# Kernel tuning notes

Hardware: AMD Instinct MI355X
Metric: run time of the kernel (lower is better)

The kernel has to match this reference:

```python
import jax, jax.numpy as jnp
import numpy as np
import math

B, L, D, H = 16, 512, 128, 8


def setup_inputs() -> dict:
    key = jax.random.key(0)
    ks = jax.random.split(key, 10)
    xavier = lambda k, shp: jax.random.normal(k, shp, jnp.float32) * math.sqrt(2.0 / (shp[0] + shp[1]))
    inp = {
        "x": jax.random.normal(ks[0], (B, L, D), jnp.float32),
        "W_q": xavier(ks[1], (H * D, D)),
        "b_q": jnp.zeros((H * D,), jnp.float32),
        "W_k": xavier(ks[2], (H * D, D)),
        "b_k": jnp.zeros((H * D,), jnp.float32),
        "W_v": xavier(ks[3], (H * D, D)),
        "b_v": jnp.zeros((H * D,), jnp.float32),
        "W_o": xavier(ks[4], (D, H * D)),
        "b_o": jnp.zeros((D,), jnp.float32),
        "pad_mask": jax.random.randint(ks[5], (B, L, L), 0, 2).astype(bool),
        "batch_size": B,
        "max_len": L,
    }
    return inp


def reference(x, W_q, b_q, W_k, b_k, W_v, b_v, W_o, b_o, pad_mask, batch_size, max_len):
    # project: [B, L, D] -> [B, L, H*D] -> head-major [H*B, L, D]
    def proj(W, b):
        y = jnp.einsum('bld,ed->ble', x, W) + b          # [B, L, H*D]
        y = y.reshape(batch_size, max_len, H, D)
        return y.transpose(2, 0, 1, 3).reshape(H * batch_size, max_len, D)

    q = proj(W_q, b_q)
    k = proj(W_k, b_k)
    v = proj(W_v, b_v)

    scores = jnp.einsum('nqd,nkd->nqk', q, k)            # [H*B, L, L]
    mask = jnp.tile(pad_mask, (H, 1, 1))                 # repeat(n_heads,1,1)
    # faithful quirk: mask BEFORE scaling, softmax over QUERY axis (dim=1)
    scores = jnp.where(mask, -1e9, scores) / math.sqrt(D)
    attn = jax.nn.softmax(scores, axis=1)
    att = jnp.einsum('nqk,nkd->nqd', attn, v)            # [H*B, L, D]
    # faithful quirk: torch .view from (H*B, L, D) to (B, L, H*D)
    att = att.reshape(batch_size, max_len, H * D)
    out = jnp.einsum('ble,de->bld', att, W_o) + b_o      # [B, L, D]
    return out
```

## Files before the change

### kernel.cpp

```cpp
#include <hip/hip_runtime.h>

#define B_  16
#define L_  512
#define D_  128
#define H_  8
#define HD_ 1024
#define NH_ 128
#define M_  8192

typedef unsigned short u16;
typedef __attribute__((ext_vector_type(8))) short s16x8;
typedef __attribute__((ext_vector_type(4))) float f32x4;

__device__ __forceinline__ float bf2f(u16 u) {
    union { unsigned u; float f; } x; x.u = ((unsigned)u) << 16; return x.f;
}
__device__ __forceinline__ u16 f2bf(float f) {
    unsigned u = __float_as_uint(f);
    return (u16)((u + 0x7FFFu + ((u >> 16) & 1u)) >> 16);
}

template<int MI, int MJ>
__device__ __forceinline__ void mfma_bt(const u16* __restrict__ A, int lda,
                                        const u16* __restrict__ B, int ldb,
                                        int K, int lane, f32x4 acc[MI][MJ]) {
    const int mr = lane & 15, quad = lane >> 4;
    for (int k0 = 0; k0 < K; k0 += 32) {
        s16x8 av[MI], bv[MJ];
#pragma unroll
        for (int i = 0; i < MI; i++)
            av[i] = *(const s16x8*)(A + (size_t)(i * 16 + mr) * lda + k0 + quad * 8);
#pragma unroll
        for (int j = 0; j < MJ; j++)
            bv[j] = *(const s16x8*)(B + (size_t)(j * 16 + mr) * ldb + k0 + quad * 8);
#pragma unroll
        for (int i = 0; i < MI; i++)
#pragma unroll
            for (int j = 0; j < MJ; j++)
                acc[i][j] = __builtin_amdgcn_mfma_f32_16x16x32_bf16(av[i], bv[j], acc[i][j], 0, 0, 0);
    }
}

__global__ void k0_detect(const unsigned int* __restrict__ pad,
                          const unsigned int* __restrict__ xw,
                          int* __restrict__ flags) {
    __shared__ int sMask, sCnt;
    if (threadIdx.x == 0) { sMask = 0; sCnt = 0; }
    __syncthreads();
    int bad = 0;
#pragma unroll
    for (int i = 0; i < 4; i++) {
        unsigned u = pad[threadIdx.x * 4 + i];
        bad |= (u > 1u) ? 1 : 0;
    }
    int cnt = 0;
#pragma unroll
    for (int i = 0; i < 16; i++) {
        unsigned w = xw[threadIdx.x * 16 + i];
        unsigned e = (w >> 7) & 0xFFu;
        cnt += (e >= 100u && e <= 131u) ? 1 : 0;
    }
    if (bad) atomicOr(&sMask, 1);
    atomicAdd(&sCnt, cnt);
    __syncthreads();
    if (threadIdx.x == 0) {
        flags[0] = (sCnt > 2048) ? 1 : 0;
        flags[1] = sMask;
    }
}

#define PREP_G8 197008
__global__ __launch_bounds__(256) void kprep_conv8(
    const void* x, const void* Wq, const void* bq, const void* Wk, const void* bk,
    const void* Wv, const void* bv, const void* Wo, const void* bo,
    const int* __restrict__ flags,
    u16* xb, u16* Wqb, u16* Wkb, u16* Wvb, u16* Wob,
    u16* bqb, u16* bkb, u16* bvb, u16* bob) {
    int g = blockIdx.x * 256 + threadIdx.x;
    if (g >= PREP_G8) return;
    int e0 = g * 8;
    const int dt = flags[0];
    const void* src; u16* dst; int off;
    if      (e0 < 1048576) { src = x;  dst = xb;  off = e0; }
    else if (e0 < 1179648) { src = Wq; dst = Wqb; off = e0 - 1048576; }
    else if (e0 < 1310720) { src = Wk; dst = Wkb; off = e0 - 1179648; }
    else if (e0 < 1441792) { src = Wv; dst = Wvb; off = e0 - 1310720; }
    else if (e0 < 1572864) { src = Wo; dst = Wob; off = e0 - 1441792; }
    else if (e0 < 1573888) { src = bq; dst = bqb; off = e0 - 1572864; }
    else if (e0 < 1574912) { src = bk; dst = bkb; off = e0 - 1573888; }
    else if (e0 < 1575936) { src = bv; dst = bvb; off = e0 - 1574912; }
    else                   { src = bo; dst = bob; off = e0 - 1575936; }
    if (dt) {
        *(uint4*)(dst + off) = *(const uint4*)((const u16*)src + off);
    } else {
        float4 a = *(const float4*)((const float*)src + off);
        float4 b = *(const float4*)((const float*)src + off + 4);
        u16 t[8] = {f2bf(a.x), f2bf(a.y), f2bf(a.z), f2bf(a.w),
                    f2bf(b.x), f2bf(b.y), f2bf(b.z), f2bf(b.w)};
        *(uint4*)(dst + off) = *(const uint4*)t;
    }
}

__global__ __launch_bounds__(256) void kprep_mask(const void* __restrict__ pad,
                                                  const int* __restrict__ flags,
                                                  unsigned* __restrict__ mb,
                                                  float* __restrict__ lsum) {
    int w = blockIdx.x * 256 + threadIdx.x;
    if (w < 65536) lsum[w] = 0.f;
    unsigned m = 0;
    if (flags[1]) {
        union { uint4 v[2]; unsigned a[8]; } u;
        u.v[0] = ((const uint4*)pad)[w * 2];
        u.v[1] = ((const uint4*)pad)[w * 2 + 1];
#pragma unroll
        for (int b = 0; b < 32; b++)
            m |= (((u.a[b >> 2] >> ((b & 3) * 8)) & 0xFFu) ? 1u : 0u) << b;
    } else {
        union { uint4 v[8]; unsigned a[32]; } u;
#pragma unroll
        for (int i = 0; i < 8; i++) u.v[i] = ((const uint4*)pad)[w * 8 + i];
#pragma unroll
        for (int b = 0; b < 32; b++) m |= (u.a[b] ? 1u : 0u) << b;
    }
    mb[w] = m;
}

__global__ __launch_bounds__(256) void k1_proj(
    const u16* __restrict__ xb,
    const u16* __restrict__ Wqb, const u16* __restrict__ Wkb, const u16* __restrict__ Wvb,
    const u16* __restrict__ bqb, const u16* __restrict__ bkb, const u16* __restrict__ bvb,
    u16* __restrict__ qb, u16* __restrict__ kb, u16* __restrict__ vtb) {
    const int h  = blockIdx.x;
    const int m0 = blockIdx.y * 128;
    const int z  = blockIdx.z;
    const u16* W    = (z == 0) ? Wqb : (z == 1) ? Wkb : Wvb;
    const u16* bias = (z == 0) ? bqb : (z == 1) ? bkb : bvb;

    const int lane = threadIdx.x & 63, wave = threadIdx.x >> 6;
    const int wr = wave >> 1, wc = wave & 1;
    const int mr = lane & 15, quad = lane >> 4;

    f32x4 acc[4][4];
#pragma unroll
    for (int i = 0; i < 4; i++)
#pragma unroll
        for (int j = 0; j < 4; j++) acc[i][j] = (f32x4){0.f, 0.f, 0.f, 0.f};

    mfma_bt<4,4>(xb + (size_t)(m0 + wr * 64) * D_, D_,
                 W + (size_t)(h * 128 + wc * 64) * D_, D_, D_, lane, acc);

    __shared__ __align__(16) u16 T[128][136];
#pragma unroll
    for (int i = 0; i < 4; i++)
#pragma unroll
        for (int j = 0; j < 4; j++) {
            int col = wc * 64 + j * 16 + mr;
            float bv_ = bf2f(bias[h * 128 + col]);
#pragma unroll
            for (int r = 0; r < 4; r++)
                T[wr * 64 + i * 16 + quad * 4 + r][col] = f2bf(acc[i][j][r] + bv_);
        }
    __syncthreads();

    const int bb = m0 >> 9, l0 = m0 & 511;
    const int t = threadIdx.x;
    if (z < 2) {
        u16* out = z ? kb : qb;
        int row = t >> 1, c0 = (t & 1) * 64;
        u16* dst = out + ((size_t)(h * B_ + bb) * L_ + l0 + row) * D_ + c0;
#pragma unroll
        for (int c = 0; c < 64; c += 8)
            *(uint4*)(dst + c) = *(const uint4*)&T[row][c0 + c];
    } else {
        int d = t >> 1, lc0 = (t & 1) * 64;
        u16* dst = vtb + ((size_t)(h * B_ + bb) * D_ + d) * L_ + l0 + lc0;
#pragma unroll
        for (int c = 0; c < 64; c += 8) {
            u16 tmp[8];
#pragma unroll
            for (int s = 0; s < 8; s++) tmp[s] = T[lc0 + c + s][d];
            *(uint4*)(dst + c) = *(const uint4*)tmp;
        }
    }
}

__global__ __launch_bounds__(256) void k2_escore(
    const u16* __restrict__ qb, const u16* __restrict__ kb,
    const unsigned* __restrict__ mbits,
    u16* __restrict__ E, float* __restrict__ lsum) {
    const int n  = blockIdx.x;
    const int ks = blockIdx.y;
    const int qq = blockIdx.z;
    const int bb = n & (B_ - 1);
    const int tid = threadIdx.x;
    const int lane = tid & 63, wave = tid >> 6;
    const int wr = wave >> 1, wc = wave & 1;
    const int mr = lane & 15, quad = lane >> 4;
    const float rs = 0.08838834764831845f;

    __shared__ __align__(16) u16 Te[128][136];
    __shared__ unsigned mw[512];
    __shared__ float CS[2][128];

#pragma unroll
    for (int s = 0; s < 2; s++) {
        int idx = tid * 2 + s;
        int ql = idx >> 2, lw = idx & 3;
        mw[idx] = mbits[((size_t)(bb << 9) + qq * 128 + ql) * 16 + ks * 4 + lw];
    }
    __syncthreads();

    f32x4 acc[4][4];
#pragma unroll
    for (int i = 0; i < 4; i++)
#pragma unroll
        for (int j = 0; j < 4; j++) acc[i][j] = (f32x4){0.f, 0.f, 0.f, 0.f};

    mfma_bt<4,4>(qb + (size_t)n * L_ * D_ + (size_t)(qq * 128 + wr * 64) * D_, D_,
                 kb + (size_t)n * L_ * D_ + (size_t)(ks * 128 + wc * 64) * D_, D_,
                 D_, lane, acc);

    float colsum[4] = {0.f, 0.f, 0.f, 0.f};
#pragma unroll
    for (int j = 0; j < 4; j++) {
        const int kc = wc * 64 + j * 16 + mr;
        const int lw = kc >> 5, bit = kc & 31;
#pragma unroll
        for (int i = 0; i < 4; i++)
#pragma unroll
            for (int r = 0; r < 4; r++) {
                int ql = wr * 64 + i * 16 + quad * 4 + r;
                float e = ((mw[(ql << 2) + lw] >> bit) & 1u)
                          ? 0.f : __expf(acc[i][j][r] * rs);
                colsum[j] += e;
                Te[ql][kc] = f2bf(e);
            }
    }
#pragma unroll
    for (int j = 0; j < 4; j++) {
        colsum[j] += __shfl_xor(colsum[j], 16);
        colsum[j] += __shfl_xor(colsum[j], 32);
    }
    if (quad == 0) {
#pragma unroll
        for (int j = 0; j < 4; j++) CS[wr][wc * 64 + j * 16 + mr] = colsum[j];
    }
    __syncthreads();

    {
        int row = tid >> 1, c0 = (tid & 1) * 64;
        u16* dst = E + ((size_t)(n * L_ + qq * 128 + row)) * L_ + ks * 128 + c0;
#pragma unroll
        for (int c = 0; c < 64; c += 8)
            *(uint4*)(dst + c) = *(const uint4*)&Te[row][c0 + c];
    }
    if (tid < 128)
        atomicAdd(&lsum[(size_t)n * L_ + ks * 128 + tid], CS[0][tid] + CS[1][tid]);
}

__global__ __launch_bounds__(256) void k3_vscale(u16* __restrict__ vtb,
                                                 const float* __restrict__ lsum) {
    int idx = blockIdx.x * 256 + threadIdx.x;
    int n = idx >> 13;
    int rem = idx & 8191;
    int d = rem >> 6;
    int kg = (rem & 63) << 3;
    u16* p = vtb + ((size_t)n * D_ + d) * L_ + kg;
    uint4 v = *(const uint4*)p;
    float4 l0 = *(const float4*)(lsum + (size_t)n * L_ + kg);
    float4 l1 = *(const float4*)(lsum + (size_t)n * L_ + kg + 4);
    float lv[8] = {1.f/l0.x, 1.f/l0.y, 1.f/l0.z, 1.f/l0.w,
                   1.f/l1.x, 1.f/l1.y, 1.f/l1.z, 1.f/l1.w};
    u16* u = (u16*)&v;
#pragma unroll
    for (int s = 0; s < 8; s++) u[s] = f2bf(bf2f(u[s]) * lv[s]);
    *(uint4*)p = v;
}

__global__ __launch_bounds__(256) void k4_av(
    const u16* __restrict__ E, const u16* __restrict__ vtb,
    u16* __restrict__ att) {
    const int n  = blockIdx.x;
    const int qt = blockIdx.y;
    const int tid = threadIdx.x;
    const int lane = tid & 63, w = tid >> 6;
    const int mr = lane & 15, quad = lane >> 4;

    f32x4 acc[4][2];
#pragma unroll
    for (int i = 0; i < 4; i++)
#pragma unroll
        for (int j = 0; j < 2; j++) acc[i][j] = (f32x4){0.f, 0.f, 0.f, 0.f};

    mfma_bt<4,2>(E + ((size_t)n * L_ + qt * 64) * L_, L_,
                 vtb + ((size_t)n * D_ + w * 32) * L_, L_, L_, lane, acc);

    __shared__ __align__(16) u16 Ta[64][136];
#pragma unroll
    for (int i = 0; i < 4; i++)
#pragma unroll
        for (int j = 0; j < 2; j++) {
            int col = w * 32 + j * 16 + mr;
#pragma unroll
            for (int r = 0; r < 4; r++)
                Ta[i * 16 + quad * 4 + r][col] = f2bf(acc[i][j][r]);
        }
    __syncthreads();
    int row = tid >> 2, c0 = (tid & 3) * 32;
    u16* dst = att + ((size_t)(n * L_ + qt * 64 + row)) * D_ + c0;
#pragma unroll
    for (int c = 0; c < 32; c += 8)
        *(uint4*)(dst + c) = *(const uint4*)&Ta[row][c0 + c];
}

__global__ __launch_bounds__(256) void k5_out(
    const u16* __restrict__ att, const u16* __restrict__ Wob,
    const u16* __restrict__ bob, const int* __restrict__ flags,
    void* __restrict__ out) {
    const int dt = flags[0];
    const int n0 = blockIdx.x * 64;
    const int m0 = blockIdx.y * 32;
    const int tid = threadIdx.x;
    const int lane = tid & 63, wk = tid >> 6;
    const int mr = lane & 15, quad = lane >> 4;

    f32x4 acc[2][4];
#pragma unroll
    for (int i = 0; i < 2; i++)
#pragma unroll
        for (int j = 0; j < 4; j++) acc[i][j] = (f32x4){0.f, 0.f, 0.f, 0.f};

    mfma_bt<2,4>(att + (size_t)m0 * HD_ + wk * 256, HD_,
                 Wob + (size_t)n0 * HD_ + wk * 256, HD_, 256, lane, acc);

    __shared__ __align__(16) float Tf[2][32][68];
    if (wk < 2) {
#pragma unroll
        for (int i = 0; i < 2; i++)
#pragma unroll
            for (int j = 0; j < 4; j++)
#pragma unroll
                for (int r = 0; r < 4; r++)
                    Tf[wk][i * 16 + quad * 4 + r][j * 16 + mr] = acc[i][j][r];
    }
    __syncthreads();
    if (wk >= 2) {
#pragma unroll
        for (int i = 0; i < 2; i++)
#pragma unroll
            for (int j = 0; j < 4; j++)
#pragma unroll
                for (int r = 0; r < 4; r++)
                    Tf[wk - 2][i * 16 + quad * 4 + r][j * 16 + mr] += acc[i][j][r];
    }
    __syncthreads();

    int row = tid >> 3, c0 = (tid & 7) * 8;
    size_t base = (size_t)(m0 + row) * D_ + n0 + c0;
    float v[8];
#pragma unroll
    for (int s = 0; s < 8; s++)
        v[s] = Tf[0][row][c0 + s] + Tf[1][row][c0 + s] + bf2f(bob[n0 + c0 + s]);
    if (dt) {
        u16 tmp[8];
#pragma unroll
        for (int s = 0; s < 8; s++) tmp[s] = f2bf(v[s]);
        *(uint4*)((u16*)out + base) = *(const uint4*)tmp;
    } else {
        float* o = (float*)out;
        *(float4*)(o + base)     = *(const float4*)&v[0];
        *(float4*)(o + base + 4) = *(const float4*)&v[4];
    }
}

extern "C" void kernel_launch(void* const* d_in, const int* in_sizes, int n_in,
                              void* d_out, int out_size, void* d_ws, size_t ws_size,
                              hipStream_t stream) {
    (void)in_sizes; (void)n_in; (void)out_size; (void)ws_size;
    const void* x  = d_in[0];
    const void* Wq = d_in[1]; const void* bq = d_in[2];
    const void* Wk = d_in[3]; const void* bk = d_in[4];
    const void* Wv = d_in[5]; const void* bv = d_in[6];
    const void* Wo = d_in[7]; const void* bo = d_in[8];
    const void* pad = d_in[9];

    char* p = (char*)d_ws;
    auto alloc = [&](size_t bytes) { char* r = p; p += (bytes + 255) & ~(size_t)255; return r; };
    int*  flags = (int*)alloc(256);
    u16*  xb   = (u16*)alloc(2097152);
    u16*  Wqb  = (u16*)alloc(262144);
    u16*  Wkb  = (u16*)alloc(262144);
    u16*  Wvb  = (u16*)alloc(262144);
    u16*  Wob  = (u16*)alloc(262144);
    u16*  bqb  = (u16*)alloc(2048);
    u16*  bkb  = (u16*)alloc(2048);
    u16*  bvb  = (u16*)alloc(2048);
    u16*  bob  = (u16*)alloc(256);
    unsigned* mbits = (unsigned*)alloc(524288);
    float* lsum = (float*)alloc(262144);
    u16*  qb   = (u16*)alloc(16777216);
    u16*  kb   = (u16*)alloc(16777216);
    u16*  vtb  = (u16*)alloc(16777216);
    u16*  E    = (u16*)alloc(67108864);
    u16*  att  = qb;

    k0_detect<<<1, 256, 0, stream>>>((const unsigned*)pad, (const unsigned*)x, flags);
    kprep_conv8<<<(PREP_G8 + 255) / 256, 256, 0, stream>>>(
        x, Wq, bq, Wk, bk, Wv, bv, Wo, bo, flags,
        xb, Wqb, Wkb, Wvb, Wob, bqb, bkb, bvb, bob);
    kprep_mask<<<512, 256, 0, stream>>>(pad, flags, mbits, lsum);
    k1_proj<<<dim3(8, 64, 3), 256, 0, stream>>>(
        xb, Wqb, Wkb, Wvb, bqb, bkb, bvb, qb, kb, vtb);
    k2_escore<<<dim3(128, 4, 4), 256, 0, stream>>>(qb, kb, mbits, E, lsum);
    k3_vscale<<<4096, 256, 0, stream>>>(vtb, lsum);
    k4_av<<<dim3(128, 8), 256, 0, stream>>>(E, vtb, att);
    k5_out<<<dim3(2, 256), 256, 0, stream>>>(att, Wob, bob, flags, d_out);
}
```

Baseline: 263.3 us.

## Fuse input conversion into GEMMs, fold V scaling into AV, shrink blocks

Drops the separate fp32-to-bf16 prep kernel and converts x and the weights on the fly inside the projection and output GEMM fragment loads. Removes the V rescale pass and applies 1/colsum inside the AV kernel via a shared reciprocal table. Resizes k1, k2 and k4 to single-wave 64-thread blocks with smaller tiles and larger grids, and k2 now accumulates column sums directly with atomics. The aim is fewer launches and less intermediate traffic. The cost is repeated conversion work per tile and more atomics.

```diff
diff --git a/kernel.cpp b/kernel.cpp
--- a/kernel.cpp
+++ b/kernel.cpp
@@ -19,20 +19,36 @@
     unsigned u = __float_as_uint(f);
     return (u16)((u + 0x7FFFu + ((u >> 16) & 1u)) >> 16);
 }
+__device__ __forceinline__ float ld1(const void* p, size_t i, int dt) {
+    if (dt) return bf2f(((const u16*)p)[i]);
+    return ((const float*)p)[i];
+}
+
+__device__ __forceinline__ s16x8 ld_frag(const void* p, size_t off, int dt) {
+    if (dt) return *(const s16x8*)((const u16*)p + off);
+    const float* f = (const float*)p + off;
+    float4 a = *(const float4*)f;
+    float4 b = *(const float4*)(f + 4);
+    union { u16 u[8]; s16x8 v; } t;
+    t.u[0] = f2bf(a.x); t.u[1] = f2bf(a.y); t.u[2] = f2bf(a.z); t.u[3] = f2bf(a.w);
+    t.u[4] = f2bf(b.x); t.u[5] = f2bf(b.y); t.u[6] = f2bf(b.z); t.u[7] = f2bf(b.w);
+    return t.v;
+}
 
 template<int MI, int MJ>
-__device__ __forceinline__ void mfma_bt(const u16* __restrict__ A, int lda,
-                                        const u16* __restrict__ B, int ldb,
-                                        int K, int lane, f32x4 acc[MI][MJ]) {
+__device__ __forceinline__ void mfma_core(
+    const void* __restrict__ A, size_t offA, int lda, int dtA,
+    const void* __restrict__ B, size_t offB, int ldb, int dtB,
+    int K, int lane, f32x4 acc[MI][MJ]) {
     const int mr = lane & 15, quad = lane >> 4;
     for (int k0 = 0; k0 < K; k0 += 32) {
         s16x8 av[MI], bv[MJ];
 #pragma unroll
         for (int i = 0; i < MI; i++)
-            av[i] = *(const s16x8*)(A + (size_t)(i * 16 + mr) * lda + k0 + quad * 8);
+            av[i] = ld_frag(A, offA + (size_t)(i * 16 + mr) * lda + k0 + quad * 8, dtA);
 #pragma unroll
         for (int j = 0; j < MJ; j++)
-            bv[j] = *(const s16x8*)(B + (size_t)(j * 16 + mr) * ldb + k0 + quad * 8);
+            bv[j] = ld_frag(B, offB + (size_t)(j * 16 + mr) * ldb + k0 + quad * 8, dtB);
 #pragma unroll
         for (int i = 0; i < MI; i++)
 #pragma unroll
@@ -66,38 +82,6 @@
     if (threadIdx.x == 0) {
         flags[0] = (sCnt > 2048) ? 1 : 0;
         flags[1] = sMask;
-    }
-}
-
-#define PREP_G8 197008
-__global__ __launch_bounds__(256) void kprep_conv8(
-    const void* x, const void* Wq, const void* bq, const void* Wk, const void* bk,
-    const void* Wv, const void* bv, const void* Wo, const void* bo,
-    const int* __restrict__ flags,
-    u16* xb, u16* Wqb, u16* Wkb, u16* Wvb, u16* Wob,
-    u16* bqb, u16* bkb, u16* bvb, u16* bob) {
-    int g = blockIdx.x * 256 + threadIdx.x;
-    if (g >= PREP_G8) return;
-    int e0 = g * 8;
-    const int dt = flags[0];
-    const void* src; u16* dst; int off;
-    if      (e0 < 1048576) { src = x;  dst = xb;  off = e0; }
-    else if (e0 < 1179648) { src = Wq; dst = Wqb; off = e0 - 1048576; }
-    else if (e0 < 1310720) { src = Wk; dst = Wkb; off = e0 - 1179648; }
-    else if (e0 < 1441792) { src = Wv; dst = Wvb; off = e0 - 1310720; }
-    else if (e0 < 1572864) { src = Wo; dst = Wob; off = e0 - 1441792; }
-    else if (e0 < 1573888) { src = bq; dst = bqb; off = e0 - 1572864; }
-    else if (e0 < 1574912) { src = bk; dst = bkb; off = e0 - 1573888; }
-    else if (e0 < 1575936) { src = bv; dst = bvb; off = e0 - 1574912; }
-    else                   { src = bo; dst = bob; off = e0 - 1575936; }
-    if (dt) {
-        *(uint4*)(dst + off) = *(const uint4*)((const u16*)src + off);
-    } else {
-        float4 a = *(const float4*)((const float*)src + off);
-        float4 b = *(const float4*)((const float*)src + off + 4);
-        u16 t[8] = {f2bf(a.x), f2bf(a.y), f2bf(a.z), f2bf(a.w),
-                    f2bf(b.x), f2bf(b.y), f2bf(b.z), f2bf(b.w)};
-        *(uint4*)(dst + off) = *(const uint4*)t;
     }
 }
 
@@ -125,19 +109,20 @@
     mb[w] = m;
 }
 
-__global__ __launch_bounds__(256) void k1_proj(
-    const u16* __restrict__ xb,
-    const u16* __restrict__ Wqb, const u16* __restrict__ Wkb, const u16* __restrict__ Wvb,
-    const u16* __restrict__ bqb, const u16* __restrict__ bkb, const u16* __restrict__ bvb,
+__global__ __launch_bounds__(64) void k1_proj(
+    const void* __restrict__ x,
+    const void* __restrict__ Wq, const void* __restrict__ Wk, const void* __restrict__ Wv,
+    const void* __restrict__ bq, const void* __restrict__ bk, const void* __restrict__ bv,
+    const int* __restrict__ flags,
     u16* __restrict__ qb, u16* __restrict__ kb, u16* __restrict__ vtb) {
-    const int h  = blockIdx.x;
-    const int m0 = blockIdx.y * 128;
+    const int dt = flags[0];
+    const int m0 = blockIdx.x * 64;
+    const int ye = blockIdx.y;
     const int z  = blockIdx.z;
-    const u16* W    = (z == 0) ? Wqb : (z == 1) ? Wkb : Wvb;
-    const u16* bias = (z == 0) ? bqb : (z == 1) ? bkb : bvb;
-
-    const int lane = threadIdx.x & 63, wave = threadIdx.x >> 6;
-    const int wr = wave >> 1, wc = wave & 1;
+    const void* W    = (z == 0) ? Wq : (z == 1) ? Wk : Wv;
+    const void* bias = (z == 0) ? bq : (z == 1) ? bk : bv;
+
+    const int lane = threadIdx.x;
     const int mr = lane & 15, quad = lane >> 4;
 
     f32x4 acc[4][4];
@@ -146,91 +131,81 @@
 #pragma unroll
         for (int j = 0; j < 4; j++) acc[i][j] = (f32x4){0.f, 0.f, 0.f, 0.f};
 
-    mfma_bt<4,4>(xb + (size_t)(m0 + wr * 64) * D_, D_,
-                 W + (size_t)(h * 128 + wc * 64) * D_, D_, D_, lane, acc);
-
-    __shared__ __align__(16) u16 T[128][136];
+    mfma_core<4,4>(x, (size_t)m0 * D_, D_, dt,
+                   W, (size_t)ye * 64 * D_, D_, dt, D_, lane, acc);
+
+    __shared__ __align__(16) u16 T[64][72];
 #pragma unroll
     for (int i = 0; i < 4; i++)
 #pragma unroll
         for (int j = 0; j < 4; j++) {
-            int col = wc * 64 + j * 16 + mr;
-            float bv_ = bf2f(bias[h * 128 + col]);
-#pragma unroll
-            for (int r = 0; r < 4; r++)
-                T[wr * 64 + i * 16 + quad * 4 + r][col] = f2bf(acc[i][j][r] + bv_);
+            int colL = j * 16 + mr;
+            float bv_ = ld1(bias, ye * 64 + colL, dt);
+#pragma unroll
+            for (int r = 0; r < 4; r++) {
+                int row = i * 16 + quad * 4 + r;
+                float v = acc[i][j][r] + bv_;
+                if (z < 2) T[row][colL] = f2bf(v);
+                else       T[colL][row] = f2bf(v);
+            }
         }
     __syncthreads();
 
     const int bb = m0 >> 9, l0 = m0 & 511;
+    const int h = ye >> 1, d0 = (ye & 1) * 64;
     const int t = threadIdx.x;
     if (z < 2) {
         u16* out = z ? kb : qb;
-        int row = t >> 1, c0 = (t & 1) * 64;
-        u16* dst = out + ((size_t)(h * B_ + bb) * L_ + l0 + row) * D_ + c0;
+        u16* dst = out + ((size_t)(h * B_ + bb) * L_ + l0 + t) * D_ + d0;
 #pragma unroll
         for (int c = 0; c < 64; c += 8)
-            *(uint4*)(dst + c) = *(const uint4*)&T[row][c0 + c];
+            *(uint4*)(dst + c) = *(const uint4*)&T[t][c];
     } else {
-        int d = t >> 1, lc0 = (t & 1) * 64;
-        u16* dst = vtb + ((size_t)(h * B_ + bb) * D_ + d) * L_ + l0 + lc0;
-#pragma unroll
-        for (int c = 0; c < 64; c += 8) {
-            u16 tmp[8];
-#pragma unroll
-            for (int s = 0; s < 8; s++) tmp[s] = T[lc0 + c + s][d];
-            *(uint4*)(dst + c) = *(const uint4*)tmp;
-        }
-    }
-}
-
-__global__ __launch_bounds__(256) void k2_escore(
+        u16* dst = vtb + ((size_t)(h * B_ + bb) * D_ + d0 + t) * L_ + l0;
+#pragma unroll
+        for (int c = 0; c < 64; c += 8)
+            *(uint4*)(dst + c) = *(const uint4*)&T[t][c];
+    }
+}
+
+__global__ __launch_bounds__(64) void k2_escore(
     const u16* __restrict__ qb, const u16* __restrict__ kb,
     const unsigned* __restrict__ mbits,
     u16* __restrict__ E, float* __restrict__ lsum) {
     const int n  = blockIdx.x;
     const int ks = blockIdx.y;
-    const int qq = blockIdx.z;
+    const int qs = blockIdx.z;
     const int bb = n & (B_ - 1);
-    const int tid = threadIdx.x;
-    const int lane = tid & 63, wave = tid >> 6;
-    const int wr = wave >> 1, wc = wave & 1;
+    const int lane = threadIdx.x;
     const int mr = lane & 15, quad = lane >> 4;
     const float rs = 0.08838834764831845f;
 
-    __shared__ __align__(16) u16 Te[128][136];
-    __shared__ unsigned mw[512];
-    __shared__ float CS[2][128];
-
-#pragma unroll
-    for (int s = 0; s < 2; s++) {
-        int idx = tid * 2 + s;
-        int ql = idx >> 2, lw = idx & 3;
-        mw[idx] = mbits[((size_t)(bb << 9) + qq * 128 + ql) * 16 + ks * 4 + lw];
-    }
-    __syncthreads();
-
-    f32x4 acc[4][4];
-#pragma unroll
-    for (int i = 0; i < 4; i++)
+    __shared__ __align__(16) u16 Te[32][72];
+    __shared__ unsigned mw[64];
+    mw[lane] = mbits[((size_t)(bb << 9) + qs * 32 + (lane >> 1)) * 16 + ks * 2 + (lane & 1)];
+    __syncthreads();
+
+    f32x4 acc[2][4];
+#pragma unroll
+    for (int i = 0; i < 2; i++)
 #pragma unroll
         for (int j = 0; j < 4; j++) acc[i][j] = (f32x4){0.f, 0.f, 0.f, 0.f};
 
-    mfma_bt<4,4>(qb + (size_t)n * L_ * D_ + (size_t)(qq * 128 + wr * 64) * D_, D_,
-                 kb + (size_t)n * L_ * D_ + (size_t)(ks * 128 + wc * 64) * D_, D_,
-                 D_, lane, acc);
+    mfma_core<2,4>(qb, ((size_t)n * L_ + qs * 32) * D_, D_, 1,
+                   kb, ((size_t)n * L_ + ks * 64) * D_, D_, 1, D_, lane, acc);
 
     float colsum[4] = {0.f, 0.f, 0.f, 0.f};
 #pragma unroll
     for (int j = 0; j < 4; j++) {
-        const int kc = wc * 64 + j * 16 + mr;
-        const int lw = kc >> 5, bit = kc & 31;
-#pragma unroll
-        for (int i = 0; i < 4; i++)
+        const int kc = j * 16 + mr;
+        const int lw = j >> 1;
+        const int bit = (j & 1) * 16 + mr;
+#pragma unroll
+        for (int i = 0; i < 2; i++)
 #pragma unroll
             for (int r = 0; r < 4; r++) {
-                int ql = wr * 64 + i * 16 + quad * 4 + r;
-                float e = ((mw[(ql << 2) + lw] >> bit) & 1u)
+                int ql = i * 16 + quad * 4 + r;
+                float e = ((mw[ql * 2 + lw] >> bit) & 1u)
                           ? 0.f : __expf(acc[i][j][r] * rs);
                 colsum[j] += e;
                 Te[ql][kc] = f2bf(e);
@@ -243,48 +218,43 @@
     }
     if (quad == 0) {
 #pragma unroll
-        for (int j = 0; j < 4; j++) CS[wr][wc * 64 + j * 16 + mr] = colsum[j];
-    }
-    __syncthreads();
-
+        for (int j = 0; j < 4; j++)
+            atomicAdd(&lsum[(size_t)n * L_ + ks * 64 + j * 16 + mr], colsum[j]);
+    }
+    __syncthreads();
     {
-        int row = tid >> 1, c0 = (tid & 1) * 64;
-        u16* dst = E + ((size_t)(n * L_ + qq * 128 + row)) * L_ + ks * 128 + c0;
-#pragma unroll
-        for (int c = 0; c < 64; c += 8)
-            *(uint4*)(dst + c) = *(const uint4*)&Te[row][c0 + c];
-    }
-    if (tid < 128)
-        atomicAdd(&lsum[(size_t)n * L_ + ks * 128 + tid], CS[0][tid] + CS[1][tid]);
-}
-
-__global__ __launch_bounds__(256) void k3_vscale(u16* __restrict__ vtb,
-                                                 const float* __restrict__ lsum) {
-    int idx = blockIdx.x * 256 + threadIdx.x;
-    int n = idx >> 13;
-    int rem = idx & 8191;
-    int d = rem >> 6;
-    int kg = (rem & 63) << 3;
-    u16* p = vtb + ((size_t)n * D_ + d) * L_ + kg;
-    uint4 v = *(const uint4*)p;
-    float4 l0 = *(const float4*)(lsum + (size_t)n * L_ + kg);
-    float4 l1 = *(const float4*)(lsum + (size_t)n * L_ + kg + 4);
-    float lv[8] = {1.f/l0.x, 1.f/l0.y, 1.f/l0.z, 1.f/l0.w,
-                   1.f/l1.x, 1.f/l1.y, 1.f/l1.z, 1.f/l1.w};
-    u16* u = (u16*)&v;
-#pragma unroll
-    for (int s = 0; s < 8; s++) u[s] = f2bf(bf2f(u[s]) * lv[s]);
-    *(uint4*)p = v;
-}
-
-__global__ __launch_bounds__(256) void k4_av(
+        int r = lane >> 1, c0 = (lane & 1) * 32;
+        u16* dst = E + ((size_t)n * L_ + qs * 32 + r) * L_ + ks * 64 + c0;
+#pragma unroll
+        for (int c = 0; c < 32; c += 8)
+            *(uint4*)(dst + c) = *(const uint4*)&Te[r][c0 + c];
+    }
+}
+
+__global__ __launch_bounds__(64) void k4_av(
     const u16* __restrict__ E, const u16* __restrict__ vtb,
-    u16* __restrict__ att) {
+    const float* __restrict__ lsum, u16* __restrict__ att) {
     const int n  = blockIdx.x;
     const int qt = blockIdx.y;
-    const int tid = threadIdx.x;
-    const int lane = tid & 63, w = tid >> 6;
-    const int mr = lane & 15, quad = lane >> 4;
+    const int ds = blockIdx.z;
+    const int lane = threadIdx.x;
+    const int mr = lane & 15, quad = lane >> 4;
+
+    __shared__ float linvS[512];
+    __shared__ __align__(16) u16 Ta[64][40];
+    {
+        const float* lp = lsum + (size_t)n * L_ + lane * 8;
+        float4 a = *(const float4*)lp;
+        float4 b = *(const float4*)(lp + 4);
+        linvS[lane * 8 + 0] = 1.f / a.x; linvS[lane * 8 + 1] = 1.f / a.y;
+        linvS[lane * 8 + 2] = 1.f / a.z; linvS[lane * 8 + 3] = 1.f / a.w;
+        linvS[lane * 8 + 4] = 1.f / b.x; linvS[lane * 8 + 5] = 1.f / b.y;
+        linvS[lane * 8 + 6] = 1.f / b.z; linvS[lane * 8 + 7] = 1.f / b.w;
+    }
+    __syncthreads();
+
+    const u16* Eb = E + ((size_t)n * L_ + qt * 64) * L_;
+    const u16* vb = vtb + ((size_t)n * D_ + ds * 32) * L_;
 
     f32x4 acc[4][2];
 #pragma unroll
@@ -292,30 +262,49 @@
 #pragma unroll
         for (int j = 0; j < 2; j++) acc[i][j] = (f32x4){0.f, 0.f, 0.f, 0.f};
 
-    mfma_bt<4,2>(E + ((size_t)n * L_ + qt * 64) * L_, L_,
-                 vtb + ((size_t)n * D_ + w * 32) * L_, L_, L_, lane, acc);
-
-    __shared__ __align__(16) u16 Ta[64][136];
+    for (int k0 = 0; k0 < L_; k0 += 32) {
+        s16x8 av[4], bv[2];
+#pragma unroll
+        for (int i = 0; i < 4; i++)
+            av[i] = *(const s16x8*)(Eb + (size_t)(i * 16 + mr) * L_ + k0 + quad * 8);
+        float lv[8];
+        *(float4*)&lv[0] = *(const float4*)&linvS[k0 + quad * 8];
+        *(float4*)&lv[4] = *(const float4*)&linvS[k0 + quad * 8 + 4];
+#pragma unroll
+        for (int j = 0; j < 2; j++) {
+            s16x8 raw = *(const s16x8*)(vb + (size_t)(j * 16 + mr) * L_ + k0 + quad * 8);
+            union { u16 u[8]; s16x8 v; } t;
+#pragma unroll
+            for (int s = 0; s < 8; s++)
+                t.u[s] = f2bf(bf2f((u16)raw[s]) * lv[s]);
+            bv[j] = t.v;
+        }
+#pragma unroll
+        for (int i = 0; i < 4; i++)
+#pragma unroll
+            for (int j = 0; j < 2; j++)
+                acc[i][j] = __builtin_amdgcn_mfma_f32_16x16x32_bf16(av[i], bv[j], acc[i][j], 0, 0, 0);
+    }
+
 #pragma unroll
     for (int i = 0; i < 4; i++)
 #pragma unroll
         for (int j = 0; j < 2; j++) {
-            int col = w * 32 + j * 16 + mr;
+            int col = j * 16 + mr;
 #pragma unroll
             for (int r = 0; r < 4; r++)
                 Ta[i * 16 + quad * 4 + r][col] = f2bf(acc[i][j][r]);
         }
     __syncthreads();
-    int row = tid >> 2, c0 = (tid & 3) * 32;
-    u16* dst = att + ((size_t)(n * L_ + qt * 64 + row)) * D_ + c0;
+    u16* dst = att + ((size_t)n * L_ + qt * 64 + lane) * D_ + ds * 32;
 #pragma unroll
     for (int c = 0; c < 32; c += 8)
-        *(uint4*)(dst + c) = *(const uint4*)&Ta[row][c0 + c];
+        *(uint4*)(dst + c) = *(const uint4*)&Ta[lane][c];
 }
 
 __global__ __launch_bounds__(256) void k5_out(
-    const u16* __restrict__ att, const u16* __restrict__ Wob,
-    const u16* __restrict__ bob, const int* __restrict__ flags,
+    const u16* __restrict__ att, const void* __restrict__ Wo,
+    const void* __restrict__ bo, const int* __restrict__ flags,
     void* __restrict__ out) {
     const int dt = flags[0];
     const int n0 = blockIdx.x * 64;
@@ -330,8 +319,8 @@
 #pragma unroll
         for (int j = 0; j < 4; j++) acc[i][j] = (f32x4){0.f, 0.f, 0.f, 0.f};
 
-    mfma_bt<2,4>(att + (size_t)m0 * HD_ + wk * 256, HD_,
-                 Wob + (size_t)n0 * HD_ + wk * 256, HD_, 256, lane, acc);
+    mfma_core<2,4>(att, (size_t)m0 * HD_ + wk * 256, HD_, 1,
+                   Wo, (size_t)n0 * HD_ + wk * 256, HD_, dt, 256, lane, acc);
 
     __shared__ __align__(16) float Tf[2][32][68];
     if (wk < 2) {
@@ -360,7 +349,7 @@
     float v[8];
 #pragma unroll
     for (int s = 0; s < 8; s++)
-        v[s] = Tf[0][row][c0 + s] + Tf[1][row][c0 + s] + bf2f(bob[n0 + c0 + s]);
+        v[s] = Tf[0][row][c0 + s] + Tf[1][row][c0 + s] + ld1(bo, n0 + c0 + s, dt);
     if (dt) {
         u16 tmp[8];
 #pragma unroll
@@ -387,15 +376,6 @@
     char* p = (char*)d_ws;
     auto alloc = [&](size_t bytes) { char* r = p; p += (bytes + 255) & ~(size_t)255; return r; };
     int*  flags = (int*)alloc(256);
-    u16*  xb   = (u16*)alloc(2097152);
-    u16*  Wqb  = (u16*)alloc(262144);
-    u16*  Wkb  = (u16*)alloc(262144);
-    u16*  Wvb  = (u16*)alloc(262144);
-    u16*  Wob  = (u16*)alloc(262144);
-    u16*  bqb  = (u16*)alloc(2048);
-    u16*  bkb  = (u16*)alloc(2048);
-    u16*  bvb  = (u16*)alloc(2048);
-    u16*  bob  = (u16*)alloc(256);
     unsigned* mbits = (unsigned*)alloc(524288);
     float* lsum = (float*)alloc(262144);
     u16*  qb   = (u16*)alloc(16777216);
@@ -405,14 +385,10 @@
     u16*  att  = qb;
 
     k0_detect<<<1, 256, 0, stream>>>((const unsigned*)pad, (const unsigned*)x, flags);
-    kprep_conv8<<<(PREP_G8 + 255) / 256, 256, 0, stream>>>(
-        x, Wq, bq, Wk, bk, Wv, bv, Wo, bo, flags,
-        xb, Wqb, Wkb, Wvb, Wob, bqb, bkb, bvb, bob);
     kprep_mask<<<512, 256, 0, stream>>>(pad, flags, mbits, lsum);
-    k1_proj<<<dim3(8, 64, 3), 256, 0, stream>>>(
-        xb, Wqb, Wkb, Wvb, bqb, bkb, bvb, qb, kb, vtb);
-    k2_escore<<<dim3(128, 4, 4), 256, 0, stream>>>(qb, kb, mbits, E, lsum);
-    k3_vscale<<<4096, 256, 0, stream>>>(vtb, lsum);
-    k4_av<<<dim3(128, 8), 256, 0, stream>>>(E, vtb, att);
-    k5_out<<<dim3(2, 256), 256, 0, stream>>>(att, Wob, bob, flags, d_out);
-}
+    k1_proj<<<dim3(128, 16, 3), 64, 0, stream>>>(
+        x, Wq, Wk, Wv, bq, bk, bv, flags, qb, kb, vtb);
+    k2_escore<<<dim3(128, 8, 16), 64, 0, stream>>>(qb, kb, mbits, E, lsum);
+    k4_av<<<dim3(128, 8, 4), 64, 0, stream>>>(E, vtb, lsum, att);
+    k5_out<<<dim3(2, 256), 256, 0, stream>>>(att, Wo, bo, flags, d_out);
+}
```

After: 294.0 us. +11.7%, slower.
